# Performance work log

Measured on AMD Instinct MI355X. Metric: run time of the kernel, lower is better.

Reference implementation:

```python
import jax, jax.numpy as jnp
import numpy as np

B, CL, QL, D = 32, 1024, 512, 256


def setup_inputs() -> dict:
    key = jax.random.key(0)
    ks = jax.random.split(key, 8)
    c = jax.random.normal(ks[0], (B, CL, D), jnp.float32)
    q = jax.random.normal(ks[1], (B, QL, D), jnp.float32)
    scale = 1.0 / np.sqrt(D)
    w_c = jax.random.normal(ks[2], (D,), jnp.float32) * scale
    b_c = jax.random.normal(ks[3], (), jnp.float32) * 0.01
    w_q = jax.random.normal(ks[4], (D,), jnp.float32) * scale
    b_q = jax.random.normal(ks[5], (), jnp.float32) * 0.01
    w_cq = jax.random.normal(ks[6], (D,), jnp.float32) * scale
    b_cq = jax.random.normal(ks[7], (), jnp.float32) * 0.01
    return {"c": c, "q": q, "w_c": w_c, "b_c": b_c, "w_q": w_q, "b_q": b_q,
            "w_cq": w_cq, "b_cq": b_cq}


def reference(c, q, w_c, b_c, w_q, b_q, w_cq, b_cq):
    # s[b,i,j] = w_c.c_i + w_q.q_j + w_cq.(c_i*q_j) + biases
    sc = c @ w_c + b_c                                   # (B, CL)
    sq = q @ w_q + b_q                                   # (B, QL)
    # The original per-j loop att_weight_cq(c * q_j) is a batched bilinear form.
    cq = jnp.einsum('bid,bjd,d->bij', c, q, w_cq) + b_cq  # (B, CL, QL)
    s = sc[:, :, None] + sq[:, None, :] + cq              # (B, CL, QL)
    a = jax.nn.softmax(s, axis=2)
    c2q_att = jnp.einsum('bij,bjd->bid', a, q)            # (B, CL, D)
    bvec = jax.nn.softmax(jnp.max(s, axis=2), axis=1)     # (B, CL)
    q2c = jnp.einsum('bi,bid->bd', bvec, c)               # (B, D)
    q2c_att = jnp.broadcast_to(q2c[:, None, :], c.shape)  # (B, CL, D)
    x = jnp.concatenate([c, c2q_att, c * c2q_att, c * q2c_att], axis=-1)
    return x
```

## Files before the change

kernel.cpp:

```cpp
#include <hip/hip_runtime.h>

#define B_  32
#define CL_ 1024
#define QL_ 512
#define D_  256

typedef _Float16 f16;
typedef __attribute__((ext_vector_type(2))) _Float16 f16x2;
typedef __attribute__((ext_vector_type(4))) _Float16 f16x4;
typedef __attribute__((ext_vector_type(8))) _Float16 f16x8;
typedef __attribute__((ext_vector_type(4))) float    f32x4;

__global__ __launch_bounds__(256) void k0_prep(const float* __restrict__ q,
                                               const float* __restrict__ w_q,
                                               f16* __restrict__ qF,
                                               f16* __restrict__ qTF,
                                               float* __restrict__ sqv) {
  __shared__ f16 q_l[64][258];
  int b = blockIdx.y, J = blockIdx.x, j0 = J * 64, tid = threadIdx.x;
  int r = tid >> 2, seg = tid & 3;
  const float* qrow = q + ((size_t)(b * QL_ + j0 + r)) * D_ + seg * 64;
  float dot = 0.f;
  #pragma unroll
  for (int u = 0; u < 16; ++u) {
    f32x4 v  = *(const f32x4*)(qrow + 4 * u);
    f32x4 wv = *(const f32x4*)(w_q + seg * 64 + 4 * u);
    f16x4 h;
    h[0] = (f16)v[0]; h[1] = (f16)v[1]; h[2] = (f16)v[2]; h[3] = (f16)v[3];
    *(f16x4*)(&q_l[r][seg * 64 + 4 * u]) = h;
    dot += v[0]*wv[0] + v[1]*wv[1] + v[2]*wv[2] + v[3]*wv[3];
  }
  dot += __shfl_xor(dot, 1, 64);
  dot += __shfl_xor(dot, 2, 64);
  if (seg == 0) sqv[b * QL_ + j0 + r] = dot;
  __syncthreads();

  const int ww = tid >> 6, l = tid & 63, g = l >> 4, l15 = l & 15;
  f16* qFb = qF + ((size_t)(b * 8 + J)) * 16384;
  #pragma unroll
  for (int t = 0; t < 8; ++t) {
    int task = ww * 8 + t;
    int dk = task >> 2, fj = task & 3;
    f16x8 v = *(const f16x8*)(&q_l[16 * fj + l15][dk * 32 + 8 * g]);
    *(f16x8*)(qFb + ((size_t)task * 64 + l) * 8) = v;
  }
  #pragma unroll
  for (int t = 0; t < 8; ++t) {
    int task = ww * 8 + t;
    int W = task >> 2, jtl = (task >> 1) & 1, fd = task & 1;
    f16x8 v;
    #pragma unroll
    for (int e = 0; e < 8; ++e)
      v[e] = q_l[32 * jtl + 8 * g + e][32 * W + 16 * fd + l15];
    *(f16x8*)(qTF + ((((size_t)(b * 8 + W) * 16 + (2 * J + jtl)) * 2 + fd) * 64 + l) * 8) = v;
  }
}

__global__ __launch_bounds__(512, 4) void k1_fused(
    const float* __restrict__ c, const f16* __restrict__ qF,
    const f16* __restrict__ qTF, const float* __restrict__ sqv,
    const float* __restrict__ w_c, const float* __restrict__ w_cq,
    f16* __restrict__ c2qh, float* __restrict__ mrow)
{
  __shared__ alignas(16) char smem[72448];
  f16 (*cw_t)[264]  = (f16 (*)[264])(smem);
  char* P_b         = smem;
  f16 (*c2q_l)[264] = (f16 (*)[264])(smem);
  float* sqv_l = (float*)(smem + 65536);
  float* wcq_l = (float*)(smem + 67584);
  float* wc_l  = (float*)(smem + 68608);
  float* scv_l = (float*)(smem + 69632);
  float (*red)[64] = (float (*)[64])(smem + 69888);
  float* mf = (float*)(smem + 71936);
  float* lf = (float*)(smem + 72192);

  const int tid = threadIdx.x;
  const int w = tid >> 6, l = tid & 63, g = l >> 4, l15 = l & 15;
  const int lin = blockIdx.x, xcd = lin & 7, slot = lin >> 3;
  const int b  = xcd * 4 + (slot >> 4);
  const int i0 = (slot & 15) * 64;

  if (tid < 256) { wcq_l[tid] = w_cq[tid]; wc_l[tid] = w_c[tid]; }
  sqv_l[tid] = sqv[b * QL_ + tid];
  __syncthreads();

  {
    int row = tid >> 3, seg = tid & 7;
    const float* crow = c + (size_t)(b * CL_ + i0 + row) * D_ + seg * 32;
    float dot = 0.f;
    #pragma unroll
    for (int u = 0; u < 8; ++u) {
      f32x4 v  = *(const f32x4*)(crow + 4 * u);
      f32x4 wv = *(const f32x4*)(wcq_l + seg * 32 + 4 * u);
      f32x4 w2 = *(const f32x4*)(wc_l  + seg * 32 + 4 * u);
      f16x4 h;
      h[0] = (f16)(v[0]*wv[0]); h[1] = (f16)(v[1]*wv[1]);
      h[2] = (f16)(v[2]*wv[2]); h[3] = (f16)(v[3]*wv[3]);
      *(f16x4*)(&cw_t[row][seg * 32 + 4 * u]) = h;
      dot += v[0]*w2[0] + v[1]*w2[1] + v[2]*w2[2] + v[3]*w2[3];
    }
    dot += __shfl_xor(dot, 1, 64); dot += __shfl_xor(dot, 2, 64);
    dot += __shfl_xor(dot, 4, 64);
    if (seg == 0) scv_l[row] = dot;
  }
  __syncthreads();

  f32x4 acc[4][4];
  #pragma unroll
  for (int fi = 0; fi < 4; ++fi)
    #pragma unroll
    for (int fj = 0; fj < 4; ++fj)
      acc[fi][fj] = (f32x4){0.f,0.f,0.f,0.f};

  const f16* qFb = qF + ((size_t)(b * 8 + w)) * 16384;
  #pragma unroll
  for (int dk = 0; dk < 8; ++dk) {
    f16x8 av[4];
    #pragma unroll
    for (int fi = 0; fi < 4; ++fi)
      av[fi] = *(const f16x8*)(&cw_t[16 * fi + l15][dk * 32 + 8 * g]);
    #pragma unroll
    for (int fj = 0; fj < 4; ++fj) {
      f16x8 bf = *(const f16x8*)(qFb + (((size_t)dk * 4 + fj) * 64 + l) * 8);
      #pragma unroll
      for (int fi = 0; fi < 4; ++fi)
        acc[fi][fj] = __builtin_amdgcn_mfma_f32_16x16x32_f16(av[fi], bf, acc[fi][fj], 0, 0, 0);
    }
  }

  #pragma unroll
  for (int fi = 0; fi < 4; ++fi) {
    #pragma unroll
    for (int r = 0; r < 4; ++r) {
      float mx = -1e30f;
      #pragma unroll
      for (int fj = 0; fj < 4; ++fj) {
        float v = acc[fi][fj][r] + sqv_l[64 * w + 16 * fj + l15];
        acc[fi][fj][r] = v;
        mx = fmaxf(mx, v);
      }
      mx = fmaxf(mx, __shfl_xor(mx, 1, 64));
      mx = fmaxf(mx, __shfl_xor(mx, 2, 64));
      mx = fmaxf(mx, __shfl_xor(mx, 4, 64));
      mx = fmaxf(mx, __shfl_xor(mx, 8, 64));
      if (l15 == 0) red[w][16 * fi + 4 * g + r] = mx;
    }
  }
  __syncthreads();
  if (tid < 64) {
    float m = red[0][tid];
    #pragma unroll
    for (int w2 = 1; w2 < 8; ++w2) m = fmaxf(m, red[w2][tid]);
    mf[tid] = m;
    mrow[b * CL_ + i0 + tid] = m + scv_l[tid];
  }
  __syncthreads();
  #pragma unroll
  for (int fi = 0; fi < 4; ++fi) {
    #pragma unroll
    for (int r = 0; r < 4; ++r) {
      float mv = mf[16 * fi + 4 * g + r];
      float s = 0.f;
      #pragma unroll
      for (int fj = 0; fj < 4; ++fj) {
        float p = __expf(acc[fi][fj][r] - mv);
        acc[fi][fj][r] = p;
        s += p;
      }
      s += __shfl_xor(s, 1, 64); s += __shfl_xor(s, 2, 64);
      s += __shfl_xor(s, 4, 64); s += __shfl_xor(s, 8, 64);
      if (l15 == 0) red[w][16 * fi + 4 * g + r] = s;
    }
  }
  __syncthreads();
  if (tid < 64) {
    float s = 0.f;
    #pragma unroll
    for (int w2 = 0; w2 < 8; ++w2) s += red[w2][tid];
    lf[tid] = 1.0f / s;
  }
  __syncthreads();

  #pragma unroll
  for (int fi = 0; fi < 4; ++fi) {
    #pragma unroll
    for (int r = 0; r < 4; ++r) {
      int row = 16 * fi + 4 * g + r;
      float inv = lf[row];
      #pragma unroll
      for (int fj = 0; fj < 4; ++fj) {
        *(f16*)(P_b + (((row << 10) + 128 * w + 32 * fj + 2 * l15) ^ ((row & 7) << 4)))
            = (f16)(acc[fi][fj][r] * inv);
      }
    }
  }
  __syncthreads();

  f32x4 o[4][2];
  #pragma unroll
  for (int fi = 0; fi < 4; ++fi) { o[fi][0] = (f32x4){0.f,0.f,0.f,0.f}; o[fi][1] = o[fi][0]; }
  const f16* qTFb = qTF + ((size_t)(b * 8 + w)) * 16384;
  #pragma unroll
  for (int jt = 0; jt < 16; ++jt) {
    f16x8 qf0 = *(const f16x8*)(qTFb + (((size_t)jt * 2 + 0) * 64 + l) * 8);
    f16x8 qf1 = *(const f16x8*)(qTFb + (((size_t)jt * 2 + 1) * 64 + l) * 8);
    #pragma unroll
    for (int fi = 0; fi < 4; ++fi) {
      int row = 16 * fi + l15;
      f16x8 pa = *(const f16x8*)(P_b + (((row << 10) + 64 * jt + 16 * g) ^ ((row & 7) << 4)));
      o[fi][0] = __builtin_amdgcn_mfma_f32_16x16x32_f16(pa, qf0, o[fi][0], 0, 0, 0);
      o[fi][1] = __builtin_amdgcn_mfma_f32_16x16x32_f16(pa, qf1, o[fi][1], 0, 0, 0);
    }
  }
  __syncthreads();

  #pragma unroll
  for (int fi = 0; fi < 4; ++fi)
    #pragma unroll
    for (int fd = 0; fd < 2; ++fd)
      #pragma unroll
      for (int r = 0; r < 4; ++r)
        c2q_l[16 * fi + 4 * g + r][32 * w + 16 * fd + l15] = (f16)o[fi][fd][r];
  __syncthreads();
  f16* dst = c2qh + ((size_t)(b * CL_ + i0)) * 256;
  #pragma unroll
  for (int s = 0; s < 4; ++s) {
    int idx = tid + 512 * s;
    int row = idx >> 5, col8 = (idx & 31) * 8;
    *(f16x8*)(dst + (size_t)row * 256 + col8) = *(const f16x8*)(&c2q_l[row][col8]);
  }
}

__global__ __launch_bounds__(256) void k2a_bvec(const float* __restrict__ mrow,
                                                float* __restrict__ bvec) {
  __shared__ float red[256];
  int b = blockIdx.x, tid = threadIdx.x;
  f32x4 v = *(const f32x4*)(mrow + b * CL_ + tid * 4);
  float mx = fmaxf(fmaxf(v[0], v[1]), fmaxf(v[2], v[3]));
  red[tid] = mx;
  __syncthreads();
  for (int s = 128; s > 0; s >>= 1) {
    if (tid < s) red[tid] = fmaxf(red[tid], red[tid + s]);
    __syncthreads();
  }
  float gmx = red[0];
  __syncthreads();
  f32x4 e;
  e[0] = __expf(v[0] - gmx); e[1] = __expf(v[1] - gmx);
  e[2] = __expf(v[2] - gmx); e[3] = __expf(v[3] - gmx);
  red[tid] = e[0] + e[1] + e[2] + e[3];
  __syncthreads();
  for (int s = 128; s > 0; s >>= 1) {
    if (tid < s) red[tid] += red[tid + s];
    __syncthreads();
  }
  float inv = 1.0f / red[0];
  e[0] *= inv; e[1] *= inv; e[2] *= inv; e[3] *= inv;
  *(f32x4*)(bvec + b * CL_ + tid * 4) = e;
}

__global__ __launch_bounds__(256) void k2b_part(const float* __restrict__ c,
                                                const float* __restrict__ bvec,
                                                float* __restrict__ part) {
  __shared__ f32x4 pl[4][64];
  int ch = blockIdx.x, b = blockIdx.y, tid = threadIdx.x;
  int ro = tid >> 6, dl = tid & 63;
  const float* cb = c + ((size_t)b * CL_ + ch * 128) * D_;
  const float* bv = bvec + b * CL_ + ch * 128;
  f32x4 acc = (f32x4){0.f, 0.f, 0.f, 0.f};
  for (int i = ro; i < 128; i += 4) {
    float wgt = bv[i];
    f32x4 v = *(const f32x4*)(cb + (size_t)i * D_ + dl * 4);
    acc[0] += wgt * v[0]; acc[1] += wgt * v[1];
    acc[2] += wgt * v[2]; acc[3] += wgt * v[3];
  }
  pl[ro][dl] = acc;
  __syncthreads();
  if (tid < 64) {
    f32x4 s = (pl[0][tid] + pl[1][tid]) + (pl[2][tid] + pl[3][tid]);
    *(f32x4*)(part + ((size_t)(b * 8 + ch)) * D_ + tid * 4) = s;
  }
}

__global__ __launch_bounds__(256) void k2c_red(const float* __restrict__ part,
                                               float* __restrict__ q2c) {
  int b = blockIdx.x, d = threadIdx.x;
  float s = 0.f;
  #pragma unroll
  for (int ch = 0; ch < 8; ++ch) s += part[((size_t)(b * 8 + ch)) * D_ + d];
  q2c[b * D_ + d] = s;
}

__global__ __launch_bounds__(256) void k4_out(const float* __restrict__ c,
                                              const f16* __restrict__ c2qh,
                                              const float* __restrict__ q2c,
                                              float* __restrict__ out) {
  size_t idx = (size_t)blockIdx.x * 256 + threadIdx.x;
  int b   = (int)(idx >> 16);
  int rem = (int)(idx & 65535);
  int i = rem >> 6, d4 = (rem & 63) * 4;
  size_t rowoff = (size_t)(b * CL_ + i);
  f32x4 cv = *(const f32x4*)(c + rowoff * D_ + d4);
  f16x4 gh = *(const f16x4*)(c2qh + rowoff * 256 + d4);
  f32x4 gv;
  gv[0] = (float)gh[0]; gv[1] = (float)gh[1];
  gv[2] = (float)gh[2]; gv[3] = (float)gh[3];
  f32x4 qv = *(const f32x4*)(q2c + b * D_ + d4);
  f32x4 p2, p3;
  p2[0] = cv[0]*gv[0]; p2[1] = cv[1]*gv[1]; p2[2] = cv[2]*gv[2]; p2[3] = cv[3]*gv[3];
  p3[0] = cv[0]*qv[0]; p3[1] = cv[1]*qv[1]; p3[2] = cv[2]*qv[2]; p3[3] = cv[3]*qv[3];
  float* ob = out + rowoff * (4 * D_) + d4;
  *(f32x4*)(ob)          = cv;
  *(f32x4*)(ob + D_)     = gv;
  *(f32x4*)(ob + 2 * D_) = p2;
  *(f32x4*)(ob + 3 * D_) = p3;
}

extern "C" void kernel_launch(void* const* d_in, const int* in_sizes, int n_in,
                              void* d_out, int out_size, void* d_ws, size_t ws_size,
                              hipStream_t stream) {
  const float* c    = (const float*)d_in[0];
  const float* q    = (const float*)d_in[1];
  const float* w_c  = (const float*)d_in[2];
  const float* w_q  = (const float*)d_in[4];
  const float* w_cq = (const float*)d_in[6];
  float* out = (float*)d_out;
  char* ws = (char*)d_ws;
  f16*   qF   = (f16*)ws;
  f16*   qTF  = (f16*)(ws + 8388608);
  float* sqv  = (float*)(ws + 16777216);
  float* mrow = (float*)(ws + 16842752);
  float* bvec = (float*)(ws + 16973824);
  float* part = (float*)(ws + 17104896);
  float* q2c  = (float*)(ws + 17367040);
  f16*   c2qh = (f16*)(ws + 17399808);

  hipLaunchKernelGGL(k0_prep,  dim3(8, 32),  dim3(256), 0, stream,
                     q, w_q, qF, qTF, sqv);
  hipLaunchKernelGGL(k1_fused, dim3(512),    dim3(512), 0, stream,
                     c, qF, qTF, sqv, w_c, w_cq, c2qh, mrow);
  hipLaunchKernelGGL(k2a_bvec, dim3(32),     dim3(256), 0, stream, mrow, bvec);
  hipLaunchKernelGGL(k2b_part, dim3(8, 32),  dim3(256), 0, stream, c, bvec, part);
  hipLaunchKernelGGL(k2c_red,  dim3(32),     dim3(256), 0, stream, part, q2c);
  hipLaunchKernelGGL(k4_out,   dim3(8192),   dim3(256), 0, stream,
                     c, c2qh, q2c, out);
}
```

Baseline: 89.40 us.

## Shrink fused attention tile to 32 rows with 4 waves and online softmax merge

Makes each k1 block handle 32 context rows using 4 waves instead of 64 rows with 8 waves, so each wave covers 128 query columns and two D-slices. Softmax max and sum are now computed in one pass per wave and merged across waves with rescaling factors, which removes two block barriers. The smaller tile cuts LDS from about 72KB to 38KB and doubles the grid to raise occupancy. In exchange, qF/qTF fragments are reread by twice as many blocks, which adds global/L2 traffic.

```diff
diff --git a/kernel.cpp b/kernel.cpp
--- a/kernel.cpp
+++ b/kernel.cpp
@@ -56,32 +56,33 @@
   }
 }
 
-__global__ __launch_bounds__(512, 4) void k1_fused(
+__global__ __launch_bounds__(256, 4) void k1_fused(
     const float* __restrict__ c, const f16* __restrict__ qF,
     const f16* __restrict__ qTF, const float* __restrict__ sqv,
     const float* __restrict__ w_c, const float* __restrict__ w_cq,
     f16* __restrict__ c2qh, float* __restrict__ mrow)
 {
-  __shared__ alignas(16) char smem[72448];
+  __shared__ alignas(16) char smem[38656];
   f16 (*cw_t)[264]  = (f16 (*)[264])(smem);
   char* P_b         = smem;
   f16 (*c2q_l)[264] = (f16 (*)[264])(smem);
-  float* sqv_l = (float*)(smem + 65536);
-  float* wcq_l = (float*)(smem + 67584);
-  float* wc_l  = (float*)(smem + 68608);
-  float* scv_l = (float*)(smem + 69632);
-  float (*red)[64] = (float (*)[64])(smem + 69888);
-  float* mf = (float*)(smem + 71936);
-  float* lf = (float*)(smem + 72192);
+  float* sqv_l = (float*)(smem + 32768);
+  float* wcq_l = (float*)(smem + 34816);
+  float* wc_l  = (float*)(smem + 35840);
+  float* scv_l = (float*)(smem + 36864);
+  float (*red_m)[32] = (float (*)[32])(smem + 36992);
+  float (*red_s)[32] = (float (*)[32])(smem + 37504);
+  float (*fac)[32]   = (float (*)[32])(smem + 38016);
 
   const int tid = threadIdx.x;
   const int w = tid >> 6, l = tid & 63, g = l >> 4, l15 = l & 15;
   const int lin = blockIdx.x, xcd = lin & 7, slot = lin >> 3;
-  const int b  = xcd * 4 + (slot >> 4);
-  const int i0 = (slot & 15) * 64;
-
-  if (tid < 256) { wcq_l[tid] = w_cq[tid]; wc_l[tid] = w_c[tid]; }
+  const int b  = xcd * 4 + (slot >> 5);
+  const int i0 = (slot & 31) * 32;
+
+  wcq_l[tid] = w_cq[tid]; wc_l[tid] = w_c[tid];
   sqv_l[tid] = sqv[b * QL_ + tid];
+  sqv_l[tid + 256] = sqv[b * QL_ + tid + 256];
   __syncthreads();
 
   {
@@ -105,127 +106,139 @@
   }
   __syncthreads();
 
-  f32x4 acc[4][4];
-  #pragma unroll
-  for (int fi = 0; fi < 4; ++fi)
-    #pragma unroll
-    for (int fj = 0; fj < 4; ++fj)
-      acc[fi][fj] = (f32x4){0.f,0.f,0.f,0.f};
-
-  const f16* qFb = qF + ((size_t)(b * 8 + w)) * 16384;
+  f32x4 acc[2][2][4];
+  #pragma unroll
+  for (int fi = 0; fi < 2; ++fi)
+    #pragma unroll
+    for (int jj = 0; jj < 2; ++jj)
+      #pragma unroll
+      for (int fj = 0; fj < 4; ++fj)
+        acc[fi][jj][fj] = (f32x4){0.f,0.f,0.f,0.f};
+
+  const f16* qFb0 = qF + ((size_t)(b * 8 + 2 * w)) * 16384;
+  const f16* qFb1 = qFb0 + 16384;
   #pragma unroll
   for (int dk = 0; dk < 8; ++dk) {
-    f16x8 av[4];
-    #pragma unroll
-    for (int fi = 0; fi < 4; ++fi)
-      av[fi] = *(const f16x8*)(&cw_t[16 * fi + l15][dk * 32 + 8 * g]);
+    f16x8 av0 = *(const f16x8*)(&cw_t[l15     ][dk * 32 + 8 * g]);
+    f16x8 av1 = *(const f16x8*)(&cw_t[16 + l15][dk * 32 + 8 * g]);
     #pragma unroll
     for (int fj = 0; fj < 4; ++fj) {
-      f16x8 bf = *(const f16x8*)(qFb + (((size_t)dk * 4 + fj) * 64 + l) * 8);
-      #pragma unroll
-      for (int fi = 0; fi < 4; ++fi)
-        acc[fi][fj] = __builtin_amdgcn_mfma_f32_16x16x32_f16(av[fi], bf, acc[fi][fj], 0, 0, 0);
-    }
-  }
-
-  #pragma unroll
-  for (int fi = 0; fi < 4; ++fi) {
+      f16x8 bf0 = *(const f16x8*)(qFb0 + (((size_t)dk * 4 + fj) * 64 + l) * 8);
+      f16x8 bf1 = *(const f16x8*)(qFb1 + (((size_t)dk * 4 + fj) * 64 + l) * 8);
+      acc[0][0][fj] = __builtin_amdgcn_mfma_f32_16x16x32_f16(av0, bf0, acc[0][0][fj], 0, 0, 0);
+      acc[1][0][fj] = __builtin_amdgcn_mfma_f32_16x16x32_f16(av1, bf0, acc[1][0][fj], 0, 0, 0);
+      acc[0][1][fj] = __builtin_amdgcn_mfma_f32_16x16x32_f16(av0, bf1, acc[0][1][fj], 0, 0, 0);
+      acc[1][1][fj] = __builtin_amdgcn_mfma_f32_16x16x32_f16(av1, bf1, acc[1][1][fj], 0, 0, 0);
+    }
+  }
+
+  #pragma unroll
+  for (int fi = 0; fi < 2; ++fi) {
     #pragma unroll
     for (int r = 0; r < 4; ++r) {
+      int row = 16 * fi + 4 * g + r;
       float mx = -1e30f;
       #pragma unroll
-      for (int fj = 0; fj < 4; ++fj) {
-        float v = acc[fi][fj][r] + sqv_l[64 * w + 16 * fj + l15];
-        acc[fi][fj][r] = v;
-        mx = fmaxf(mx, v);
-      }
+      for (int jj = 0; jj < 2; ++jj)
+        #pragma unroll
+        for (int fj = 0; fj < 4; ++fj) {
+          float v = acc[fi][jj][fj][r] + sqv_l[128 * w + 64 * jj + 16 * fj + l15];
+          acc[fi][jj][fj][r] = v;
+          mx = fmaxf(mx, v);
+        }
       mx = fmaxf(mx, __shfl_xor(mx, 1, 64));
       mx = fmaxf(mx, __shfl_xor(mx, 2, 64));
       mx = fmaxf(mx, __shfl_xor(mx, 4, 64));
       mx = fmaxf(mx, __shfl_xor(mx, 8, 64));
-      if (l15 == 0) red[w][16 * fi + 4 * g + r] = mx;
-    }
-  }
-  __syncthreads();
-  if (tid < 64) {
-    float m = red[0][tid];
-    #pragma unroll
-    for (int w2 = 1; w2 < 8; ++w2) m = fmaxf(m, red[w2][tid]);
-    mf[tid] = m;
-    mrow[b * CL_ + i0 + tid] = m + scv_l[tid];
-  }
-  __syncthreads();
-  #pragma unroll
-  for (int fi = 0; fi < 4; ++fi) {
-    #pragma unroll
-    for (int r = 0; r < 4; ++r) {
-      float mv = mf[16 * fi + 4 * g + r];
       float s = 0.f;
       #pragma unroll
-      for (int fj = 0; fj < 4; ++fj) {
-        float p = __expf(acc[fi][fj][r] - mv);
-        acc[fi][fj][r] = p;
-        s += p;
-      }
+      for (int jj = 0; jj < 2; ++jj)
+        #pragma unroll
+        for (int fj = 0; fj < 4; ++fj) {
+          float p = __expf(acc[fi][jj][fj][r] - mx);
+          acc[fi][jj][fj][r] = p;
+          s += p;
+        }
       s += __shfl_xor(s, 1, 64); s += __shfl_xor(s, 2, 64);
       s += __shfl_xor(s, 4, 64); s += __shfl_xor(s, 8, 64);
-      if (l15 == 0) red[w][16 * fi + 4 * g + r] = s;
-    }
-  }
-  __syncthreads();
-  if (tid < 64) {
-    float s = 0.f;
-    #pragma unroll
-    for (int w2 = 0; w2 < 8; ++w2) s += red[w2][tid];
-    lf[tid] = 1.0f / s;
-  }
-  __syncthreads();
-
-  #pragma unroll
-  for (int fi = 0; fi < 4; ++fi) {
+      if (l15 == 0) { red_m[w][row] = mx; red_s[w][row] = s; }
+    }
+  }
+  __syncthreads();
+  if (tid < 32) {
+    float m0 = red_m[0][tid], m1 = red_m[1][tid];
+    float m2 = red_m[2][tid], m3 = red_m[3][tid];
+    float m = fmaxf(fmaxf(m0, m1), fmaxf(m2, m3));
+    float e0 = __expf(m0 - m), e1 = __expf(m1 - m);
+    float e2 = __expf(m2 - m), e3 = __expf(m3 - m);
+    float stot = red_s[0][tid] * e0 + red_s[1][tid] * e1
+               + red_s[2][tid] * e2 + red_s[3][tid] * e3;
+    float inv = 1.0f / stot;
+    fac[0][tid] = e0 * inv; fac[1][tid] = e1 * inv;
+    fac[2][tid] = e2 * inv; fac[3][tid] = e3 * inv;
+    mrow[b * CL_ + i0 + tid] = m + scv_l[tid];
+  }
+  __syncthreads();
+
+  #pragma unroll
+  for (int fi = 0; fi < 2; ++fi) {
     #pragma unroll
     for (int r = 0; r < 4; ++r) {
       int row = 16 * fi + 4 * g + r;
-      float inv = lf[row];
-      #pragma unroll
-      for (int fj = 0; fj < 4; ++fj) {
-        *(f16*)(P_b + (((row << 10) + 128 * w + 32 * fj + 2 * l15) ^ ((row & 7) << 4)))
-            = (f16)(acc[fi][fj][r] * inv);
-      }
-    }
-  }
-  __syncthreads();
-
-  f32x4 o[4][2];
-  #pragma unroll
-  for (int fi = 0; fi < 4; ++fi) { o[fi][0] = (f32x4){0.f,0.f,0.f,0.f}; o[fi][1] = o[fi][0]; }
-  const f16* qTFb = qTF + ((size_t)(b * 8 + w)) * 16384;
+      float f = fac[w][row];
+      #pragma unroll
+      for (int jj = 0; jj < 2; ++jj)
+        #pragma unroll
+        for (int fj = 0; fj < 4; ++fj) {
+          int col = 256 * w + 128 * jj + 32 * fj + 2 * l15;
+          *(f16*)(P_b + (((row << 10) + col) ^ ((row & 7) << 4)))
+              = (f16)(acc[fi][jj][fj][r] * f);
+        }
+    }
+  }
+  __syncthreads();
+
+  f32x4 o[2][2][2];
+  #pragma unroll
+  for (int fi = 0; fi < 2; ++fi)
+    #pragma unroll
+    for (int Wl = 0; Wl < 2; ++Wl)
+      #pragma unroll
+      for (int fd = 0; fd < 2; ++fd)
+        o[fi][Wl][fd] = (f32x4){0.f,0.f,0.f,0.f};
+  const f16* qT0 = qTF + ((size_t)(b * 8 + 2 * w)) * 16384;
+  const f16* qT1 = qT0 + 16384;
   #pragma unroll
   for (int jt = 0; jt < 16; ++jt) {
-    f16x8 qf0 = *(const f16x8*)(qTFb + (((size_t)jt * 2 + 0) * 64 + l) * 8);
-    f16x8 qf1 = *(const f16x8*)(qTFb + (((size_t)jt * 2 + 1) * 64 + l) * 8);
-    #pragma unroll
-    for (int fi = 0; fi < 4; ++fi) {
-      int row = 16 * fi + l15;
-      f16x8 pa = *(const f16x8*)(P_b + (((row << 10) + 64 * jt + 16 * g) ^ ((row & 7) << 4)));
-      o[fi][0] = __builtin_amdgcn_mfma_f32_16x16x32_f16(pa, qf0, o[fi][0], 0, 0, 0);
-      o[fi][1] = __builtin_amdgcn_mfma_f32_16x16x32_f16(pa, qf1, o[fi][1], 0, 0, 0);
-    }
-  }
-  __syncthreads();
-
-  #pragma unroll
-  for (int fi = 0; fi < 4; ++fi)
-    #pragma unroll
-    for (int fd = 0; fd < 2; ++fd)
-      #pragma unroll
-      for (int r = 0; r < 4; ++r)
-        c2q_l[16 * fi + 4 * g + r][32 * w + 16 * fd + l15] = (f16)o[fi][fd][r];
+    f16x8 pa0 = *(const f16x8*)(P_b + ((((l15     ) << 10) + 64 * jt + 16 * g) ^ (((l15     ) & 7) << 4)));
+    f16x8 pa1 = *(const f16x8*)(P_b + ((((16 + l15) << 10) + 64 * jt + 16 * g) ^ (((16 + l15) & 7) << 4)));
+    #pragma unroll
+    for (int fd = 0; fd < 2; ++fd) {
+      f16x8 qf0 = *(const f16x8*)(qT0 + (((size_t)jt * 2 + fd) * 64 + l) * 8);
+      f16x8 qf1 = *(const f16x8*)(qT1 + (((size_t)jt * 2 + fd) * 64 + l) * 8);
+      o[0][0][fd] = __builtin_amdgcn_mfma_f32_16x16x32_f16(pa0, qf0, o[0][0][fd], 0, 0, 0);
+      o[1][0][fd] = __builtin_amdgcn_mfma_f32_16x16x32_f16(pa1, qf0, o[1][0][fd], 0, 0, 0);
+      o[0][1][fd] = __builtin_amdgcn_mfma_f32_16x16x32_f16(pa0, qf1, o[0][1][fd], 0, 0, 0);
+      o[1][1][fd] = __builtin_amdgcn_mfma_f32_16x16x32_f16(pa1, qf1, o[1][1][fd], 0, 0, 0);
+    }
+  }
+  __syncthreads();
+
+  #pragma unroll
+  for (int fi = 0; fi < 2; ++fi)
+    #pragma unroll
+    for (int Wl = 0; Wl < 2; ++Wl)
+      #pragma unroll
+      for (int fd = 0; fd < 2; ++fd)
+        #pragma unroll
+        for (int r = 0; r < 4; ++r)
+          c2q_l[16 * fi + 4 * g + r][64 * w + 32 * Wl + 16 * fd + l15]
+              = (f16)o[fi][Wl][fd][r];
   __syncthreads();
   f16* dst = c2qh + ((size_t)(b * CL_ + i0)) * 256;
   #pragma unroll
   for (int s = 0; s < 4; ++s) {
-    int idx = tid + 512 * s;
+    int idx = tid + 256 * s;
     int row = idx >> 5, col8 = (idx & 31) * 8;
     *(f16x8*)(dst + (size_t)row * 256 + col8) = *(const f16x8*)(&c2q_l[row][col8]);
   }
@@ -337,7 +350,7 @@
 
   hipLaunchKernelGGL(k0_prep,  dim3(8, 32),  dim3(256), 0, stream,
                      q, w_q, qF, qTF, sqv);
-  hipLaunchKernelGGL(k1_fused, dim3(512),    dim3(512), 0, stream,
+  hipLaunchKernelGGL(k1_fused, dim3(1024),   dim3(256), 0, stream,
                      c, qF, qTF, sqv, w_c, w_cq, c2qh, mrow);
   hipLaunchKernelGGL(k2a_bvec, dim3(32),     dim3(256), 0, stream, mrow, bvec);
   hipLaunchKernelGGL(k2b_part, dim3(8, 32),  dim3(256), 0, stream, c, bvec, part);
```

After: 103.3 us. 15.5% more time.
